# Kernel tuning notes

Measured on AMD Instinct MI355X. Metric: run time of the kernel, lower is better.

## Reference

```python
import jax, jax.numpy as jnp
import numpy as np

EPS = 1e-5  # torch BatchNorm1d default eps

# BinActive: sign forward, straight-through estimator backward (grad clipped where |x|>1)
@jax.custom_vjp
def bin_active(x):
    return jnp.sign(x)

def _ba_fwd(x):
    return jnp.sign(x), x

def _ba_bwd(x, g):
    return (g * (jnp.abs(x) <= 1.0).astype(g.dtype),)

bin_active.defvjp(_ba_fwd, _ba_bwd)

# XNOR-style weight binarization: sign(W) * mean(|W|) per output column, STE backward
@jax.custom_vjp
def bin_weight(w):
    alpha = jnp.mean(jnp.abs(w), axis=0, keepdims=True)  # [1, out]
    return jnp.sign(w) * alpha

def _bw_fwd(w):
    alpha = jnp.mean(jnp.abs(w), axis=0, keepdims=True)
    return jnp.sign(w) * alpha, w

def _bw_bwd(w, g):
    return (g * (jnp.abs(w) <= 1.0).astype(g.dtype),)

bin_weight.defvjp(_bw_fwd, _bw_bwd)


def setup_inputs() -> dict:
    key = jax.random.key(0)
    ks = jax.random.split(key, 8)
    N, E, IN, H, OUT = 100000, 1600000, 256, 128, 40
    x = jax.random.normal(ks[0], (N, IN), dtype=jnp.float32)
    edge_index = jax.random.randint(ks[1], (2, E), 0, N, dtype=jnp.int64)
    W0 = jax.random.normal(ks[2], (IN, H), dtype=jnp.float32) * (2.0 / IN) ** 0.5
    b0 = jnp.zeros((H,), dtype=jnp.float32)
    W1 = jax.random.normal(ks[3], (H, H), dtype=jnp.float32) * (2.0 / H) ** 0.5
    b1 = jnp.zeros((H,), dtype=jnp.float32)
    W2 = jax.random.normal(ks[4], (H, OUT), dtype=jnp.float32) * (2.0 / H) ** 0.5
    b2 = jnp.zeros((OUT,), dtype=jnp.float32)
    return {"x": x, "edge_index": edge_index, "W0": W0, "b0": b0,
            "W1": W1, "b1": b1, "W2": W2, "b2": b2}


def reference(x, edge_index, W0, b0, W1, b1, W2, b2):
    n = x.shape[0]
    loop = jnp.arange(n, dtype=edge_index.dtype)
    src = jnp.concatenate([edge_index[0], loop])  # add self loops (GCN norm)
    dst = jnp.concatenate([edge_index[1], loop])
    deg = jax.ops.segment_sum(jnp.ones_like(src, dtype=x.dtype), dst, num_segments=n)
    dinv = jnp.where(deg > 0, deg ** -0.5, 0.0)
    norm = (dinv[src] * dinv[dst])[:, None]  # [E+N, 1]

    # BatchNorm1d(affine=False), training-mode batch statistics (biased var)
    mu = jnp.mean(x, axis=0)
    var = jnp.var(x, axis=0)
    h = (x - mu) * jax.lax.rsqrt(var + EPS)

    for W, b in ((W0, b0), (W1, b1), (W2, b2)):
        h = bin_active(h)                       # sign binarize (dropout skipped: eval)
        h = h @ bin_weight(W)                   # binary-weight linear
        h = jax.ops.segment_sum(h[src] * norm, dst, num_segments=n) + b  # D^-1/2 (A+I) D^-1/2 agg
    return jax.nn.log_softmax(h, axis=1)
```

## Files before the change

kernel.cpp:

```cpp
#include <hip/hip_runtime.h>
#include <math.h>

#define IN_DIM 256
#define HD 128
#define OUT_DIM 40
#define S2_STRIDE 64
#define NB_CS 2048
#define NB_WP 74

__global__ __launch_bounds__(256) void k_init(int* deg, float* muacc, int N) {
    int i = blockIdx.x * 256 + threadIdx.x;
    if (i < N) deg[i] = 1;
    if (blockIdx.x == 0 && threadIdx.x < 256) muacc[threadIdx.x] = 0.f;
}

__global__ __launch_bounds__(256) void k_fuse1(const float* __restrict__ x, int N,
                                               float* __restrict__ muacc,
                                               const int* __restrict__ ei, int E, int* deg,
                                               int* __restrict__ rank,
                                               const float* __restrict__ W0,
                                               const float* __restrict__ W1,
                                               const float* __restrict__ W2,
                                               unsigned long long* W0p,
                                               unsigned long long* W1p,
                                               unsigned long long* W2p,
                                               float* aS0, float* aS1, float* aS2) {
    __shared__ float lds[256];
    int b = blockIdx.x, tid = threadIdx.x;
    if (b < NB_CS) {
        size_t F4 = (size_t)N * (IN_DIM / 4);
        size_t stride = (size_t)NB_CS * 256;
        float a0 = 0.f, a1 = 0.f, a2 = 0.f, a3 = 0.f;
        const float4* x4 = (const float4*)x;
        size_t i = (size_t)b * 256 + tid;
        for (; i + stride < F4; i += 2 * stride) {
            float4 v = x4[i];
            float4 w = x4[i + stride];
            a0 += v.x + w.x; a1 += v.y + w.y; a2 += v.z + w.z; a3 += v.w + w.w;
        }
        if (i < F4) {
            float4 v = x4[i];
            a0 += v.x; a1 += v.y; a2 += v.z; a3 += v.w;
        }
        lds[tid] = 0.f;
        __syncthreads();
        int c0 = (tid * 4) & 255;
        atomicAdd(&lds[c0], a0);
        atomicAdd(&lds[c0 + 1], a1);
        atomicAdd(&lds[c0 + 2], a2);
        atomicAdd(&lds[c0 + 3], a3);
        __syncthreads();
        atomicAdd(&muacc[tid], lds[tid]);
    } else if (b < NB_CS + NB_WP) {
        int b2 = b - NB_CS;
        int lane = tid & 63, w = tid >> 6;
        if (b2 < 32) {
            int j = b2 * 4 + w;
            float asum = 0.f;
            unsigned long long words[4];
            #pragma unroll
            for (int q = 0; q < 4; ++q) {
                float v = W0[(size_t)(4 * lane + q) * HD + j];
                asum += fabsf(v);
                words[q] = __ballot(v < 0.f);
            }
            #pragma unroll
            for (int off = 32; off; off >>= 1) asum += __shfl_xor(asum, off);
            if (lane == 0) {
                aS0[j] = 2.f * asum / 256.f;
                #pragma unroll
                for (int q = 0; q < 4; ++q) W0p[j * 4 + q] = words[q];
            }
        } else if (b2 < 64) {
            int j = (b2 - 32) * 4 + w;
            int fl = lane & 15, kk = lane >> 4;
            float asum = 0.f;
            unsigned long long words[2];
            #pragma unroll
            for (int q = 0; q < 2; ++q) {
                float v = W1[(size_t)(fl * 8 + 4 * q + kk) * HD + j];
                asum += fabsf(v);
                words[q] = __ballot(v < 0.f);
            }
            #pragma unroll
            for (int off = 32; off; off >>= 1) asum += __shfl_xor(asum, off);
            if (lane == 0) {
                aS1[j] = 2.f * asum / 128.f;
                W1p[j * 2 + 0] = words[0];
                W1p[j * 2 + 1] = words[1];
            }
        } else {
            int j = (b2 - 64) * 4 + w;
            int fl = lane & 15, kk = lane >> 4;
            if (j < OUT_DIM) {
                float asum = 0.f;
                unsigned long long words[2];
                #pragma unroll
                for (int q = 0; q < 2; ++q) {
                    float v = W2[(size_t)(fl * 8 + 4 * q + kk) * OUT_DIM + j];
                    asum += fabsf(v);
                    words[q] = __ballot(v < 0.f);
                }
                #pragma unroll
                for (int off = 32; off; off >>= 1) asum += __shfl_xor(asum, off);
                if (lane == 0) {
                    aS2[j] = 2.f * asum / 128.f;
                    W2p[j * 2 + 0] = words[0];
                    W2p[j * 2 + 1] = words[1];
                }
            }
        }
    } else {
        int e = (b - NB_CS - NB_WP) * 256 + tid;
        if (e < E) {
            int old = atomicAdd(&deg[ei[E + e]], 1);
            rank[e] = old - 1;
        }
    }
}

__global__ __launch_bounds__(256) void k_bp(const int* __restrict__ deg, int N, int* bp) {
    __shared__ int sm[256];
    int i = blockIdx.x * 256 + threadIdx.x;
    sm[threadIdx.x] = (i < N) ? (deg[i] - 1) : 0;
    __syncthreads();
    for (int off = 128; off; off >>= 1) {
        if (threadIdx.x < off) sm[threadIdx.x] += sm[threadIdx.x + off];
        __syncthreads();
    }
    if (threadIdx.x == 0) bp[blockIdx.x] = sm[0];
}

__global__ __launch_bounds__(512) void k_scanbp(const int* __restrict__ bp, int NB, int* bps) {
    __shared__ int sm[512];
    int t = threadIdx.x;
    int v = (t < NB) ? bp[t] : 0;
    sm[t] = v;
    __syncthreads();
    for (int off = 1; off < 512; off <<= 1) {
        int add = (t >= off) ? sm[t - off] : 0;
        __syncthreads();
        sm[t] += add;
        __syncthreads();
    }
    if (t < NB) bps[t] = sm[t] - v;
}

__global__ __launch_bounds__(256) void k_rowptr(const int* __restrict__ deg,
                                                const int* __restrict__ bps, int N, int E,
                                                int* row_ptr, float* dinv) {
    __shared__ int wsum[4];
    int t = threadIdx.x, lane = t & 63, w = t >> 6;
    int i = blockIdx.x * 256 + t;
    int c = (i < N) ? (deg[i] - 1) : 0;
    int v = c;
    #pragma unroll
    for (int off = 1; off < 64; off <<= 1) {
        int n = __shfl_up(v, off);
        if (lane >= off) v += n;
    }
    if (lane == 63) wsum[w] = v;
    __syncthreads();
    int wo = 0;
    for (int k = 0; k < w; ++k) wo += wsum[k];
    int excl = bps[blockIdx.x] + wo + v - c;
    if (i < N) {
        row_ptr[i] = excl;
        dinv[i] = (float)(1.0 / sqrt((double)deg[i]));
    }
    if (blockIdx.x == 0 && t == 0) row_ptr[N] = E;
}

__global__ __launch_bounds__(256) void k_fuse2(const int* __restrict__ ei, int E,
                                               const int* __restrict__ rowp,
                                               const int* __restrict__ rank,
                                               int* __restrict__ cs, int nbScat,
                                               const float* __restrict__ x,
                                               const float* __restrict__ muacc, float inv_n,
                                               const unsigned long long* __restrict__ W0p,
                                               unsigned char* __restrict__ S0, int N) {
    __shared__ unsigned long long w0s[128 * 4];
    int b = blockIdx.x, tid = threadIdx.x;
    if (b < nbScat) {
        int e = b * 256 + tid;
        if (e >= E) return;
        int s = ei[e];
        int d = ei[E + e];
        int pos = rowp[d] + rank[e];
        __builtin_nontemporal_store(s, &cs[pos]);
    } else {
        w0s[tid] = W0p[tid];
        w0s[tid + 256] = W0p[tid + 256];
        __syncthreads();
        int lane = tid & 63;
        int row = (b - nbScat) * 4 + (tid >> 6);
        if (row >= N) return;
        float4 xv = ((const float4*)(x + (size_t)row * IN_DIM))[lane];
        float4 ms = ((const float4*)muacc)[lane];
        unsigned long long xw[4];
        xw[0] = __ballot(xv.x < ms.x * inv_n);
        xw[1] = __ballot(xv.y < ms.y * inv_n);
        xw[2] = __ballot(xv.z < ms.z * inv_n);
        xw[3] = __ballot(xv.w < ms.w * inv_n);
        unsigned int pack = 0;
        #pragma unroll
        for (int t2 = 0; t2 < 2; ++t2) {
            int j = 2 * lane + t2;
            const unsigned long long* wc = &w0s[j * 4];
            int dd = __popcll(xw[0] ^ wc[0]) + __popcll(xw[1] ^ wc[1]) +
                     __popcll(xw[2] ^ wc[2]) + __popcll(xw[3] ^ wc[3]);
            int S = IN_DIM - 2 * dd;
            int s8 = S >> 1;
            if (s8 > 127) s8 = 127;
            pack |= ((unsigned int)(s8 + 128) & 0xffu) << (8 * t2);
        }
        *(unsigned short*)(S0 + (size_t)row * HD + 2 * lane) = (unsigned short)pack;
    }
}

template <int OUTC>
__global__ __launch_bounds__(256) void k_agg_mm(const unsigned char* __restrict__ Sin,
                                                const int* __restrict__ row_ptr,
                                                const int* __restrict__ cs,
                                                const float* __restrict__ dinv,
                                                const float* __restrict__ alphaS,
                                                const float* __restrict__ bias,
                                                const unsigned long long* __restrict__ Wnp,
                                                unsigned char* __restrict__ Sout, int N) {
    __shared__ unsigned long long wsm[OUTC * 2];
    int tid = threadIdx.x;
    for (int i = tid; i < OUTC * 2; i += 256) wsm[i] = Wnp[i];
    __syncthreads();
    int lane = tid & 63;
    int d = blockIdx.x * 4 + (tid >> 6);
    if (d >= N) return;
    int sub = lane >> 4;
    int fl  = lane & 15;
    float acc[8];
    #pragma unroll
    for (int k = 0; k < 8; ++k) acc[k] = 0.f;
    float dvd = dinv[d];
    if (sub == 0) {
        float nrm = dvd * dvd;
        unsigned long long r = *(const unsigned long long*)(Sin + (size_t)d * HD + fl * 8);
        unsigned int lo = (unsigned int)r, hi = (unsigned int)(r >> 32);
        #pragma unroll
        for (int k = 0; k < 4; ++k) {
            acc[k]     = fmaf(nrm, (float)((lo >> (8 * k)) & 0xffu) - 128.f, acc[k]);
            acc[k + 4] = fmaf(nrm, (float)((hi >> (8 * k)) & 0xffu) - 128.f, acc[k + 4]);
        }
    }
    int e0 = row_ptr[d], e1 = row_ptr[d + 1];
    int len = e1 - e0;
    int chunk = (len + 3) >> 2;
    int ce0 = e0 + sub * chunk;
    int ce1 = min(ce0 + chunk, e1);
    int e = ce0;
    for (; e + 3 < ce1; e += 4) {
        int sa = cs[e], sb = cs[e + 1], sc = cs[e + 2], sd = cs[e + 3];
        unsigned long long ra = *(const unsigned long long*)(Sin + (size_t)sa * HD + fl * 8);
        unsigned long long rb = *(const unsigned long long*)(Sin + (size_t)sb * HD + fl * 8);
        unsigned long long rc = *(const unsigned long long*)(Sin + (size_t)sc * HD + fl * 8);
        unsigned long long rd = *(const unsigned long long*)(Sin + (size_t)sd * HD + fl * 8);
        float na = dinv[sa] * dvd, nb = dinv[sb] * dvd;
        float nc = dinv[sc] * dvd, nd = dinv[sd] * dvd;
        unsigned int la = (unsigned int)ra, ha = (unsigned int)(ra >> 32);
        unsigned int lb = (unsigned int)rb, hb = (unsigned int)(rb >> 32);
        unsigned int lc = (unsigned int)rc, hc = (unsigned int)(rc >> 32);
        unsigned int ld = (unsigned int)rd, hd2 = (unsigned int)(rd >> 32);
        #pragma unroll
        for (int k = 0; k < 4; ++k) {
            acc[k]     = fmaf(na, (float)((la >> (8 * k)) & 0xffu) - 128.f, acc[k]);
            acc[k + 4] = fmaf(na, (float)((ha >> (8 * k)) & 0xffu) - 128.f, acc[k + 4]);
            acc[k]     = fmaf(nb, (float)((lb >> (8 * k)) & 0xffu) - 128.f, acc[k]);
            acc[k + 4] = fmaf(nb, (float)((hb >> (8 * k)) & 0xffu) - 128.f, acc[k + 4]);
            acc[k]     = fmaf(nc, (float)((lc >> (8 * k)) & 0xffu) - 128.f, acc[k]);
            acc[k + 4] = fmaf(nc, (float)((hc >> (8 * k)) & 0xffu) - 128.f, acc[k + 4]);
            acc[k]     = fmaf(nd, (float)((ld >> (8 * k)) & 0xffu) - 128.f, acc[k]);
            acc[k + 4] = fmaf(nd, (float)((hd2 >> (8 * k)) & 0xffu) - 128.f, acc[k + 4]);
        }
    }
    for (; e < ce1; ++e) {
        int s = cs[e];
        unsigned long long r = *(const unsigned long long*)(Sin + (size_t)s * HD + fl * 8);
        float nrm = dinv[s] * dvd;
        unsigned int lo = (unsigned int)r, hi = (unsigned int)(r >> 32);
        #pragma unroll
        for (int k = 0; k < 4; ++k) {
            acc[k]     = fmaf(nrm, (float)((lo >> (8 * k)) & 0xffu) - 128.f, acc[k]);
            acc[k + 4] = fmaf(nrm, (float)((hi >> (8 * k)) & 0xffu) - 128.f, acc[k + 4]);
        }
    }
    #pragma unroll
    for (int k = 0; k < 8; ++k) {
        acc[k] += __shfl_xor(acc[k], 16);
        acc[k] += __shfl_xor(acc[k], 32);
    }
    unsigned int m8 = 0;
    #pragma unroll
    for (int k = 0; k < 8; ++k) {
        int f = fl * 8 + k;
        float v = alphaS[f] * acc[k] + bias[f];
        if (v < 0.f) m8 |= (1u << k);
    }
    unsigned long long x0 = 0, x1 = 0;
    #pragma unroll
    for (int k = 0; k < 4; ++k) {
        unsigned long long bk = __ballot((m8 >> k) & 1u);
        x0 |= (bk & 0xffffULL) << (16 * k);
    }
    #pragma unroll
    for (int k = 4; k < 8; ++k) {
        unsigned long long bk = __ballot((m8 >> k) & 1u);
        x1 |= (bk & 0xffffULL) << (16 * (k - 4));
    }
    if (OUTC == 128) {
        unsigned int pack = 0;
        #pragma unroll
        for (int t2 = 0; t2 < 2; ++t2) {
            int j = 2 * lane + t2;
            int dd = __popcll(x0 ^ wsm[j * 2]) + __popcll(x1 ^ wsm[j * 2 + 1]);
            int S = HD - 2 * dd;
            pack |= ((unsigned int)((S >> 1) + 128) & 0xffu) << (8 * t2);
        }
        *(unsigned short*)(Sout + (size_t)d * HD + 2 * lane) = (unsigned short)pack;
    } else {
        int p8 = 128;
        if (lane < OUTC) {
            int dd = __popcll(x0 ^ wsm[lane * 2]) + __popcll(x1 ^ wsm[lane * 2 + 1]);
            p8 = ((HD - 2 * dd) >> 1) + 128;
        }
        Sout[(size_t)d * S2_STRIDE + lane] = (unsigned char)p8;
    }
}

__global__ __launch_bounds__(256) void k_agg_out(const unsigned char* __restrict__ S2,
                                                 const int* __restrict__ row_ptr,
                                                 const int* __restrict__ cs,
                                                 const float* __restrict__ dinv,
                                                 const float* __restrict__ alphaS2,
                                                 const float* __restrict__ b2,
                                                 float* __restrict__ out, int N) {
    int tid = threadIdx.x, lane = tid & 63;
    int d = blockIdx.x * 4 + (tid >> 6);
    if (d >= N) return;
    int sub = lane >> 4;
    int fl  = lane & 15;
    float acc[4] = {0.f, 0.f, 0.f, 0.f};
    float dvd = dinv[d];
    if (sub == 0) {
        float nrm = dvd * dvd;
        unsigned int r4 = *(const unsigned int*)(S2 + (size_t)d * S2_STRIDE + fl * 4);
        #pragma unroll
        for (int k = 0; k < 4; ++k)
            acc[k] = fmaf(nrm, (float)((r4 >> (8 * k)) & 0xffu) - 128.f, acc[k]);
    }
    int e0 = row_ptr[d], e1 = row_ptr[d + 1];
    int len = e1 - e0;
    int chunk = (len + 3) >> 2;
    int ce0 = e0 + sub * chunk;
    int ce1 = min(ce0 + chunk, e1);
    int e = ce0;
    for (; e + 3 < ce1; e += 4) {
        int sa = cs[e], sb = cs[e + 1], sc = cs[e + 2], sd = cs[e + 3];
        unsigned int ra = *(const unsigned int*)(S2 + (size_t)sa * S2_STRIDE + fl * 4);
        unsigned int rb = *(const unsigned int*)(S2 + (size_t)sb * S2_STRIDE + fl * 4);
        unsigned int rc = *(const unsigned int*)(S2 + (size_t)sc * S2_STRIDE + fl * 4);
        unsigned int rd = *(const unsigned int*)(S2 + (size_t)sd * S2_STRIDE + fl * 4);
        float na = dinv[sa] * dvd, nb = dinv[sb] * dvd;
        float nc = dinv[sc] * dvd, nd = dinv[sd] * dvd;
        #pragma unroll
        for (int k = 0; k < 4; ++k) {
            acc[k] = fmaf(na, (float)((ra >> (8 * k)) & 0xffu) - 128.f, acc[k]);
            acc[k] = fmaf(nb, (float)((rb >> (8 * k)) & 0xffu) - 128.f, acc[k]);
            acc[k] = fmaf(nc, (float)((rc >> (8 * k)) & 0xffu) - 128.f, acc[k]);
            acc[k] = fmaf(nd, (float)((rd >> (8 * k)) & 0xffu) - 128.f, acc[k]);
        }
    }
    for (; e < ce1; ++e) {
        int s = cs[e];
        unsigned int r4 = *(const unsigned int*)(S2 + (size_t)s * S2_STRIDE + fl * 4);
        float nrm = dinv[s] * dvd;
        #pragma unroll
        for (int k = 0; k < 4; ++k)
            acc[k] = fmaf(nrm, (float)((r4 >> (8 * k)) & 0xffu) - 128.f, acc[k]);
    }
    #pragma unroll
    for (int k = 0; k < 4; ++k) {
        acc[k] += __shfl_xor(acc[k], 16);
        acc[k] += __shfl_xor(acc[k], 32);
    }
    float h[4];
    float mymax = -INFINITY;
    #pragma unroll
    for (int k = 0; k < 4; ++k) {
        int f = fl * 4 + k;
        h[k] = (f < OUT_DIM) ? (alphaS2[f] * acc[k] + b2[f]) : -INFINITY;
        mymax = fmaxf(mymax, h[k]);
    }
    #pragma unroll
    for (int off = 1; off < 16; off <<= 1) mymax = fmaxf(mymax, __shfl_xor(mymax, off));
    float s4 = 0.f;
    #pragma unroll
    for (int k = 0; k < 4; ++k) {
        if (fl * 4 + k < OUT_DIM) s4 += expf(h[k] - mymax);
    }
    #pragma unroll
    for (int off = 1; off < 16; off <<= 1) s4 += __shfl_xor(s4, off);
    float lse = mymax + logf(s4);
    if (sub == 0 && fl < OUT_DIM / 4) {
        float4 o;
        o.x = h[0] - lse; o.y = h[1] - lse; o.z = h[2] - lse; o.w = h[3] - lse;
        *(float4*)(out + (size_t)d * OUT_DIM + fl * 4) = o;
    }
}

extern "C" void kernel_launch(void* const* d_in, const int* in_sizes, int n_in,
                              void* d_out, int out_size, void* d_ws, size_t ws_size,
                              hipStream_t stream) {
    const float* x  = (const float*)d_in[0];
    const int*   ei = (const int*)d_in[1];
    const float* W0 = (const float*)d_in[2];
    const float* b0 = (const float*)d_in[3];
    const float* W1 = (const float*)d_in[4];
    const float* b1 = (const float*)d_in[5];
    const float* W2 = (const float*)d_in[6];
    const float* b2 = (const float*)d_in[7];
    float* out = (float*)d_out;

    int N = in_sizes[0] / IN_DIM;
    int E = in_sizes[1] / 2;

    char* ws = (char*)d_ws;
    size_t off = 0;
    auto alloc = [&](size_t bytes) -> void* {
        off = (off + 255) & ~(size_t)255;
        void* p = (void*)(ws + off);
        off += bytes;
        return p;
    };
    float* muacc  = (float*)alloc(256 * 4);
    int*   deg    = (int*)alloc((size_t)N * 4);
    float* dinv   = (float*)alloc((size_t)N * 4);
    int*   rowp   = (int*)alloc(((size_t)N + 1) * 4);
    int*   bp     = (int*)alloc(512 * 4);
    int*   bps    = (int*)alloc(512 * 4);
    int*   rank   = (int*)alloc((size_t)E * 4);
    int*   cs     = (int*)alloc((size_t)E * 4);
    unsigned char* S0 = (unsigned char*)alloc((size_t)N * HD);
    unsigned char* S1 = (unsigned char*)alloc((size_t)N * HD);
    unsigned char* S2 = (unsigned char*)alloc((size_t)N * S2_STRIDE);
    unsigned long long* W0p = (unsigned long long*)alloc(128 * 4 * 8);
    unsigned long long* W1p = (unsigned long long*)alloc(128 * 2 * 8);
    unsigned long long* W2p = (unsigned long long*)alloc(40 * 2 * 8);
    float* aS0 = (float*)alloc(128 * 4);
    float* aS1 = (float*)alloc(128 * 4);
    float* aS2 = (float*)alloc(40 * 4);

    int nb256 = (N + 255) / 256;
    int ebl = (E + 255) / 256;
    float inv_n = 1.0f / (float)N;

    k_init<<<dim3(nb256), dim3(256), 0, stream>>>(deg, muacc, N);
    k_fuse1<<<dim3(NB_CS + NB_WP + ebl), dim3(256), 0, stream>>>(
        x, N, muacc, ei, E, deg, rank, W0, W1, W2, W0p, W1p, W2p, aS0, aS1, aS2);
    k_bp<<<dim3(nb256), dim3(256), 0, stream>>>(deg, N, bp);
    k_scanbp<<<dim3(1), dim3(512), 0, stream>>>(bp, nb256, bps);
    k_rowptr<<<dim3(nb256), dim3(256), 0, stream>>>(deg, bps, N, E, rowp, dinv);

    int nb4 = (N + 3) / 4;
    k_fuse2<<<dim3(ebl + nb4), dim3(256), 0, stream>>>(
        ei, E, rowp, rank, cs, ebl, x, muacc, inv_n, W0p, S0, N);
    k_agg_mm<128><<<dim3(nb4), dim3(256), 0, stream>>>(S0, rowp, cs, dinv, aS0, b0, W1p, S1, N);
    k_agg_mm<40><<<dim3(nb4), dim3(256), 0, stream>>>(S1, rowp, cs, dinv, aS1, b1, W2p, S2, N);
    k_agg_out<<<dim3(nb4), dim3(256), 0, stream>>>(S2, rowp, cs, dinv, aS2, b2, out, N);
    (void)out_size; (void)ws_size; (void)n_in;
}
```

Measured before the change: 554.1 us.

## Make column mean deterministic, init deg via memset, use fixed-point aggregation

The per-block column sums are now written to a partial buffer and reduced by a single-block kernel, instead of using LDS and global float atomics. The degree init kernel is replaced by a memset, with degree offsets adjusted. The hidden-layer aggregation now accumulates in 64-bit fixed point instead of float FMAs, which makes the sign decisions deterministic. The cost is an extra kernel launch, a scratch buffer and 64-bit integer multiply-adds in the hot gather loop.

After: 590.3 us. 6.5% more time.

```diff
diff --git a/kernel.cpp b/kernel.cpp
--- a/kernel.cpp
+++ b/kernel.cpp
@@ -8,23 +8,17 @@
 #define NB_CS 2048
 #define NB_WP 74
 
-__global__ __launch_bounds__(256) void k_init(int* deg, float* muacc, int N) {
-    int i = blockIdx.x * 256 + threadIdx.x;
-    if (i < N) deg[i] = 1;
-    if (blockIdx.x == 0 && threadIdx.x < 256) muacc[threadIdx.x] = 0.f;
-}
-
-__global__ __launch_bounds__(256) void k_fuse1(const float* __restrict__ x, int N,
-                                               float* __restrict__ muacc,
-                                               const int* __restrict__ ei, int E, int* deg,
-                                               int* __restrict__ rank,
-                                               const float* __restrict__ W0,
-                                               const float* __restrict__ W1,
-                                               const float* __restrict__ W2,
-                                               unsigned long long* W0p,
-                                               unsigned long long* W1p,
-                                               unsigned long long* W2p,
-                                               float* aS0, float* aS1, float* aS2) {
+__global__ __launch_bounds__(256) void k_big1(const float* __restrict__ x, int N,
+                                              float* __restrict__ part,
+                                              const int* __restrict__ ei, int E, int* deg,
+                                              int* __restrict__ rank,
+                                              const float* __restrict__ W0,
+                                              const float* __restrict__ W1,
+                                              const float* __restrict__ W2,
+                                              unsigned long long* W0p,
+                                              unsigned long long* W1p,
+                                              unsigned long long* W2p,
+                                              float* aS0, float* aS1, float* aS2) {
     __shared__ float lds[256];
     int b = blockIdx.x, tid = threadIdx.x;
     if (b < NB_CS) {
@@ -45,12 +39,17 @@
         lds[tid] = 0.f;
         __syncthreads();
         int c0 = (tid * 4) & 255;
-        atomicAdd(&lds[c0], a0);
-        atomicAdd(&lds[c0 + 1], a1);
-        atomicAdd(&lds[c0 + 2], a2);
-        atomicAdd(&lds[c0 + 3], a3);
-        __syncthreads();
-        atomicAdd(&muacc[tid], lds[tid]);
+        #pragma unroll
+        for (int p = 0; p < 4; ++p) {
+            if ((tid >> 6) == p) {
+                lds[c0]     += a0;
+                lds[c0 + 1] += a1;
+                lds[c0 + 2] += a2;
+                lds[c0 + 3] += a3;
+            }
+            __syncthreads();
+        }
+        part[(size_t)b * 256 + tid] = lds[tid];
     } else if (b < NB_CS + NB_WP) {
         int b2 = b - NB_CS;
         int lane = tid & 63, w = tid >> 6;
@@ -114,15 +113,28 @@
         int e = (b - NB_CS - NB_WP) * 256 + tid;
         if (e < E) {
             int old = atomicAdd(&deg[ei[E + e]], 1);
-            rank[e] = old - 1;
-        }
-    }
+            rank[e] = old;
+        }
+    }
+}
+
+__global__ __launch_bounds__(256) void k_mured(const float* __restrict__ part,
+                                               float* __restrict__ muacc) {
+    int t = threadIdx.x;
+    float s0 = 0.f, s1 = 0.f, s2 = 0.f, s3 = 0.f;
+    for (int b = 0; b < NB_CS; b += 4) {
+        s0 += part[(size_t)(b + 0) * 256 + t];
+        s1 += part[(size_t)(b + 1) * 256 + t];
+        s2 += part[(size_t)(b + 2) * 256 + t];
+        s3 += part[(size_t)(b + 3) * 256 + t];
+    }
+    muacc[t] = (s0 + s1) + (s2 + s3);
 }
 
 __global__ __launch_bounds__(256) void k_bp(const int* __restrict__ deg, int N, int* bp) {
     __shared__ int sm[256];
     int i = blockIdx.x * 256 + threadIdx.x;
-    sm[threadIdx.x] = (i < N) ? (deg[i] - 1) : 0;
+    sm[threadIdx.x] = (i < N) ? deg[i] : 0;
     __syncthreads();
     for (int off = 128; off; off >>= 1) {
         if (threadIdx.x < off) sm[threadIdx.x] += sm[threadIdx.x + off];
@@ -152,7 +164,7 @@
     __shared__ int wsum[4];
     int t = threadIdx.x, lane = t & 63, w = t >> 6;
     int i = blockIdx.x * 256 + t;
-    int c = (i < N) ? (deg[i] - 1) : 0;
+    int c = (i < N) ? deg[i] : 0;
     int v = c;
     #pragma unroll
     for (int off = 1; off < 64; off <<= 1) {
@@ -166,7 +178,7 @@
     int excl = bps[blockIdx.x] + wo + v - c;
     if (i < N) {
         row_ptr[i] = excl;
-        dinv[i] = (float)(1.0 / sqrt((double)deg[i]));
+        dinv[i] = (float)(1.0 / sqrt((double)(deg[i] + 1)));
     }
     if (blockIdx.x == 0 && t == 0) row_ptr[N] = E;
 }
@@ -236,18 +248,19 @@
     if (d >= N) return;
     int sub = lane >> 4;
     int fl  = lane & 15;
-    float acc[8];
-    #pragma unroll
-    for (int k = 0; k < 8; ++k) acc[k] = 0.f;
+    const float FSC = 1073741824.f;
+    long long acc[8];
+    #pragma unroll
+    for (int k = 0; k < 8; ++k) acc[k] = 0;
     float dvd = dinv[d];
     if (sub == 0) {
-        float nrm = dvd * dvd;
+        int q = (int)(dvd * dvd * FSC + 0.5f);
         unsigned long long r = *(const unsigned long long*)(Sin + (size_t)d * HD + fl * 8);
         unsigned int lo = (unsigned int)r, hi = (unsigned int)(r >> 32);
         #pragma unroll
         for (int k = 0; k < 4; ++k) {
-            acc[k]     = fmaf(nrm, (float)((lo >> (8 * k)) & 0xffu) - 128.f, acc[k]);
-            acc[k + 4] = fmaf(nrm, (float)((hi >> (8 * k)) & 0xffu) - 128.f, acc[k + 4]);
+            acc[k]     += (long long)q * ((int)((lo >> (8 * k)) & 0xffu) - 128);
+            acc[k + 4] += (long long)q * ((int)((hi >> (8 * k)) & 0xffu) - 128);
         }
     }
     int e0 = row_ptr[d], e1 = row_ptr[d + 1];
@@ -262,33 +275,35 @@
         unsigned long long rb = *(const unsigned long long*)(Sin + (size_t)sb * HD + fl * 8);
         unsigned long long rc = *(const unsigned long long*)(Sin + (size_t)sc * HD + fl * 8);
         unsigned long long rd = *(const unsigned long long*)(Sin + (size_t)sd * HD + fl * 8);
-        float na = dinv[sa] * dvd, nb = dinv[sb] * dvd;
-        float nc = dinv[sc] * dvd, nd = dinv[sd] * dvd;
+        int qa = (int)(dinv[sa] * dvd * FSC + 0.5f);
+        int qb = (int)(dinv[sb] * dvd * FSC + 0.5f);
+        int qc = (int)(dinv[sc] * dvd * FSC + 0.5f);
+        int qd = (int)(dinv[sd] * dvd * FSC + 0.5f);
         unsigned int la = (unsigned int)ra, ha = (unsigned int)(ra >> 32);
         unsigned int lb = (unsigned int)rb, hb = (unsigned int)(rb >> 32);
         unsigned int lc = (unsigned int)rc, hc = (unsigned int)(rc >> 32);
         unsigned int ld = (unsigned int)rd, hd2 = (unsigned int)(rd >> 32);
         #pragma unroll
         for (int k = 0; k < 4; ++k) {
-            acc[k]     = fmaf(na, (float)((la >> (8 * k)) & 0xffu) - 128.f, acc[k]);
-            acc[k + 4] = fmaf(na, (float)((ha >> (8 * k)) & 0xffu) - 128.f, acc[k + 4]);
-            acc[k]     = fmaf(nb, (float)((lb >> (8 * k)) & 0xffu) - 128.f, acc[k]);
-            acc[k + 4] = fmaf(nb, (float)((hb >> (8 * k)) & 0xffu) - 128.f, acc[k + 4]);
-            acc[k]     = fmaf(nc, (float)((lc >> (8 * k)) & 0xffu) - 128.f, acc[k]);
-            acc[k + 4] = fmaf(nc, (float)((hc >> (8 * k)) & 0xffu) - 128.f, acc[k + 4]);
-            acc[k]     = fmaf(nd, (float)((ld >> (8 * k)) & 0xffu) - 128.f, acc[k]);
-            acc[k + 4] = fmaf(nd, (float)((hd2 >> (8 * k)) & 0xffu) - 128.f, acc[k + 4]);
+            acc[k]     += (long long)qa * ((int)((la >> (8 * k)) & 0xffu) - 128);
+            acc[k + 4] += (long long)qa * ((int)((ha >> (8 * k)) & 0xffu) - 128);
+            acc[k]     += (long long)qb * ((int)((lb >> (8 * k)) & 0xffu) - 128);
+            acc[k + 4] += (long long)qb * ((int)((hb >> (8 * k)) & 0xffu) - 128);
+            acc[k]     += (long long)qc * ((int)((lc >> (8 * k)) & 0xffu) - 128);
+            acc[k + 4] += (long long)qc * ((int)((hc >> (8 * k)) & 0xffu) - 128);
+            acc[k]     += (long long)qd * ((int)((ld >> (8 * k)) & 0xffu) - 128);
+            acc[k + 4] += (long long)qd * ((int)((hd2 >> (8 * k)) & 0xffu) - 128);
         }
     }
     for (; e < ce1; ++e) {
         int s = cs[e];
         unsigned long long r = *(const unsigned long long*)(Sin + (size_t)s * HD + fl * 8);
-        float nrm = dinv[s] * dvd;
+        int q = (int)(dinv[s] * dvd * FSC + 0.5f);
         unsigned int lo = (unsigned int)r, hi = (unsigned int)(r >> 32);
         #pragma unroll
         for (int k = 0; k < 4; ++k) {
-            acc[k]     = fmaf(nrm, (float)((lo >> (8 * k)) & 0xffu) - 128.f, acc[k]);
-            acc[k + 4] = fmaf(nrm, (float)((hi >> (8 * k)) & 0xffu) - 128.f, acc[k + 4]);
+            acc[k]     += (long long)q * ((int)((lo >> (8 * k)) & 0xffu) - 128);
+            acc[k + 4] += (long long)q * ((int)((hi >> (8 * k)) & 0xffu) - 128);
         }
     }
     #pragma unroll
@@ -300,7 +315,8 @@
     #pragma unroll
     for (int k = 0; k < 8; ++k) {
         int f = fl * 8 + k;
-        float v = alphaS[f] * acc[k] + bias[f];
+        float fv = (float)acc[k] * 9.313225746154785e-10f;
+        float v = alphaS[f] * fv + bias[f];
         if (v < 0.f) m8 |= (1u << k);
     }
     unsigned long long x0 = 0, x1 = 0;
@@ -440,6 +456,7 @@
         return p;
     };
     float* muacc  = (float*)alloc(256 * 4);
+    float* part   = (float*)alloc((size_t)NB_CS * 256 * 4);
     int*   deg    = (int*)alloc((size_t)N * 4);
     float* dinv   = (float*)alloc((size_t)N * 4);
     int*   rowp   = (int*)alloc(((size_t)N + 1) * 4);
@@ -459,18 +476,22 @@
 
     int nb256 = (N + 255) / 256;
     int ebl = (E + 255) / 256;
+    int nb4 = (N + 3) / 4;
     float inv_n = 1.0f / (float)N;
 
-    k_init<<<dim3(nb256), dim3(256), 0, stream>>>(deg, muacc, N);
-    k_fuse1<<<dim3(NB_CS + NB_WP + ebl), dim3(256), 0, stream>>>(
-        x, N, muacc, ei, E, deg, rank, W0, W1, W2, W0p, W1p, W2p, aS0, aS1, aS2);
+    hipMemsetAsync(deg, 0, (size_t)N * 4, stream);
+
+    k_big1<<<dim3(NB_CS + NB_WP + ebl), dim3(256), 0, stream>>>(
+        x, N, part, ei, E, deg, rank, W0, W1, W2, W0p, W1p, W2p, aS0, aS1, aS2);
+    k_mured<<<dim3(1), dim3(256), 0, stream>>>(part, muacc);
+
     k_bp<<<dim3(nb256), dim3(256), 0, stream>>>(deg, N, bp);
     k_scanbp<<<dim3(1), dim3(512), 0, stream>>>(bp, nb256, bps);
     k_rowptr<<<dim3(nb256), dim3(256), 0, stream>>>(deg, bps, N, E, rowp, dinv);
 
-    int nb4 = (N + 3) / 4;
     k_fuse2<<<dim3(ebl + nb4), dim3(256), 0, stream>>>(
         ei, E, rowp, rank, cs, ebl, x, muacc, inv_n, W0p, S0, N);
+
     k_agg_mm<128><<<dim3(nb4), dim3(256), 0, stream>>>(S0, rowp, cs, dinv, aS0, b0, W1p, S1, N);
     k_agg_mm<40><<<dim3(nb4), dim3(256), 0, stream>>>(S1, rowp, cs, dinv, aS1, b1, W2p, S2, N);
     k_agg_out<<<dim3(nb4), dim3(256), 0, stream>>>(S2, rowp, cs, dinv, aS2, b2, out, N);
```
